# Kernel optimization log

Measured on AMD Instinct MI355X. Metric: run time of the kernel, lower is better.

## Reference

```python
import jax, jax.numpy as jnp
import numpy as np

B, T, L = 4096, 26, 4      # batch, num sparse tables, bag size (multi-hot)
N_ROWS, M = 100000, 64     # rows per table, embedding dim
LN_BOT = [13, 512, 256, 64]
LN_TOP = [415, 512, 256, 1]


def _mlp_params(key, ln):
    Ws, bs = [], []
    for i in range(len(ln) - 1):
        n, m = ln[i], ln[i + 1]
        key, k1, k2 = jax.random.split(key, 3)
        Ws.append(jax.random.normal(k1, (m, n), jnp.float32) * np.sqrt(2.0 / (m + n)))
        bs.append(jax.random.normal(k2, (m,), jnp.float32) * np.sqrt(1.0 / m))
    return Ws, bs


def setup_inputs() -> dict:
    key = jax.random.key(0)
    k_dense, k_idx, k_emb, k_bot, k_top = jax.random.split(key, 5)
    dense_x = jax.random.normal(k_dense, (B, LN_BOT[0]), jnp.float32)
    sparse_idx = jax.random.randint(k_idx, (B, T, L), 0, N_ROWS, jnp.int64 if jax.config.jax_enable_x64 else jnp.int32)
    # per-table uniform init U(-1/sqrt(n), 1/sqrt(n)); all tables same size -> stacked
    bound = np.sqrt(1.0 / N_ROWS)
    emb_tables = jax.random.uniform(k_emb, (T, N_ROWS, M), jnp.float32, -bound, bound)
    bw, bb = _mlp_params(k_bot, LN_BOT)
    tw, tb = _mlp_params(k_top, LN_TOP)
    return {
        "dense_x": dense_x, "sparse_idx": sparse_idx, "emb_tables": emb_tables,
        "bot_W0": bw[0], "bot_b0": bb[0], "bot_W1": bw[1], "bot_b1": bb[1],
        "bot_W2": bw[2], "bot_b2": bb[2],
        "top_W0": tw[0], "top_b0": tb[0], "top_W1": tw[1], "top_b1": tb[1],
        "top_W2": tw[2], "top_b2": tb[2],
    }


def _dlrm_forward(dense_x, sparse_idx, emb_tables, bot, top):
    # bottom MLP (all ReLU; sigmoid_layer index not hit for bottom)
    x = dense_x
    for W, b in bot:
        x = jax.nn.relu(x @ W.T + b)                       # [B, 64] at the end
    # apply_emb: per-table EmbeddingBag(mode='sum'): gather L rows, sum-pool
    # emb_tables: [T, N, M], sparse_idx: [B, T, L] -> E: [B, T, M]
    E = jax.vmap(lambda tab, ix: tab[ix].sum(axis=1), in_axes=(0, 1), out_axes=1)(
        emb_tables, sparse_idx)
    # dot interaction: concat bottom output with pooled embeddings
    Tcat = jnp.concatenate([x[:, None, :], E], axis=1)     # [B, T+1, M]
    Z = jnp.einsum("bim,bjm->bij", Tcat, Tcat)             # [B, T+1, T+1]
    li, lj = np.tril_indices(T + 1, k=-1)                  # strictly lower triangle
    Zflat = Z[:, li, lj]                                   # [B, (T+1)T/2]
    R = jnp.concatenate([x, Zflat], axis=1)                # [B, 415]
    # top MLP: ReLU hidden, Sigmoid on last layer
    h = R
    for i, (W, b) in enumerate(top):
        h = h @ W.T + b
        h = jax.nn.sigmoid(h) if i == len(top) - 1 else jax.nn.relu(h)
    return h                                               # [B, 1]


def reference(dense_x, sparse_idx, emb_tables,
              bot_W0, bot_b0, bot_W1, bot_b1, bot_W2, bot_b2,
              top_W0, top_b0, top_W1, top_b1, top_W2, top_b2):
    bot = [(bot_W0, bot_b0), (bot_W1, bot_b1), (bot_W2, bot_b2)]
    top = [(top_W0, top_b0), (top_W1, top_b1), (top_W2, top_b2)]
    return _dlrm_forward(dense_x, sparse_idx, emb_tables, bot, top)
```

## Files before the change

### kernel.cpp

```cpp
#include <hip/hip_runtime.h>
#include <hip/hip_bf16.h>
#include <cstddef>
#include <cstdint>

#define BATCH 4096
#define TT 26
#define LL 4
#define NROWS 100000
#define MM 64
#define RSTR 512

typedef __attribute__((ext_vector_type(8))) short bf16x8;
typedef __attribute__((ext_vector_type(4))) float f32x4;
typedef __attribute__((ext_vector_type(16))) float f32x16;

#define AS1 __attribute__((address_space(1)))
#define AS3 __attribute__((address_space(3)))

__device__ __forceinline__ void gload_lds16(const void* g, void* l) {
    __builtin_amdgcn_global_load_lds((const AS1 unsigned int*)g,
                                     (AS3 unsigned int*)l, 16, 0, 0);
}

__device__ __forceinline__ float bu2f(unsigned short u) {
    unsigned int x = (unsigned int)u << 16;
    float f; __builtin_memcpy(&f, &x, 4); return f;
}

#define CONVB 2112
__global__ __launch_bounds__(256) void gather_conv_kernel(
    const int* __restrict__ idx, const float* __restrict__ emb,
    const float* __restrict__ bw1, const float* __restrict__ bw2,
    const float* __restrict__ tw0, const float* __restrict__ tw1,
    __hip_bfloat16* __restrict__ bw1b, __hip_bfloat16* __restrict__ bw2b,
    __hip_bfloat16* __restrict__ tw0b, __hip_bfloat16* __restrict__ tw1b,
    unsigned short* __restrict__ E)
{
    __shared__ int sidx[TT * LL];
    const int tid = threadIdx.x;
    if (blockIdx.x < CONVB) {
        int i = blockIdx.x * 256 + tid;
        if (i < 131072) {
            bw1b[i] = __float2bfloat16(bw1[i]);
        } else if (i < 147456) {
            int j = i - 131072; bw2b[j] = __float2bfloat16(bw2[j]);
        } else if (i < 409600) {
            int j = i - 147456; int n = j >> 9, k = j & 511;
            tw0b[j] = __float2bfloat16(k < 415 ? tw0[n * 415 + k] : 0.f);
        } else {
            int j = i - 409600; tw1b[j] = __float2bfloat16(tw1[j]);
        }
        return;
    }
    const int b = blockIdx.x - CONVB;
    const int lane = tid & 63;
    const int w = tid >> 6;
    if (tid < TT * LL) sidx[tid] = idx[(size_t)b * (TT * LL) + tid];
    __syncthreads();

    float v[7][4];
#pragma unroll
    for (int rr = 0; rr < 7; rr++) {
        int t = rr * 4 + w;
        if (t < TT) {
            const float* tab = emb + (size_t)t * NROWS * MM + lane;
#pragma unroll
            for (int l = 0; l < LL; l++)
                v[rr][l] = tab[(size_t)sidx[t * LL + l] * MM];
        }
    }
#pragma unroll
    for (int rr = 0; rr < 7; rr++) {
        int t = rr * 4 + w;
        if (t < TT) {
            float s = v[rr][0] + v[rr][1] + v[rr][2] + v[rr][3];
            __hip_bfloat16 hv = __float2bfloat16(s);
            E[(size_t)b * (TT * MM) + t * MM + lane] = *(unsigned short*)&hv;
        }
    }
}

__global__ __launch_bounds__(256) void bottom_mlp_kernel(
    const float* __restrict__ dense, const float* __restrict__ bw0,
    const float* __restrict__ bb0,
    const __hip_bfloat16* __restrict__ w1b, const float* __restrict__ bb1,
    const __hip_bfloat16* __restrict__ w2b, const float* __restrict__ bb2,
    __hip_bfloat16* __restrict__ R)
{
    __shared__ float W0f[512 * 13];
    __shared__ float dL[16 * 13];
    __shared__ __align__(16) char x1L[16 * 1024];
    __shared__ __align__(16) char x2L[16 * 512];
    const int tid = threadIdx.x;
    const int lane = tid & 63;
    const int w = tid >> 6;
    const int b0 = blockIdx.x * 16;

    for (int i = tid; i < 512 * 13; i += 256) W0f[i] = bw0[i];
    if (tid < 208) dL[tid] = dense[(size_t)b0 * 13 + tid];
    __syncthreads();

    {
        const int m = tid & 15;
        float dv[13];
#pragma unroll
        for (int k = 0; k < 13; k++) dv[k] = dL[m * 13 + k];
#pragma unroll
        for (int j = 0; j < 32; j++) {
            int n = (tid >> 4) + j * 16;
            float s = bb0[n];
#pragma unroll
            for (int k = 0; k < 13; k++) s = fmaf(dv[k], W0f[n * 13 + k], s);
            __hip_bfloat16 hv = __float2bfloat16(fmaxf(s, 0.f));
            *(short*)(x1L + m * 1024 + ((n * 2) ^ ((m & 7) << 4))) = *(short*)&hv;
        }
    }
    __syncthreads();

    const int fr = lane & 15;
    const int fh = lane >> 4;

    {
        f32x4 acc1[4] = {};
#pragma unroll
        for (int kf = 0; kf < 16; kf++) {
            bf16x8 af = *(const bf16x8*)(x1L + fr * 1024 + ((kf * 64 + fh * 16) ^ ((fr & 7) << 4)));
#pragma unroll
            for (int nf = 0; nf < 4; nf++) {
                int n = w * 64 + nf * 16 + fr;
                bf16x8 bf = *(const bf16x8*)((const short*)w1b + (size_t)n * 512 + kf * 32 + fh * 8);
                acc1[nf] = __builtin_amdgcn_mfma_f32_16x16x32_bf16(af, bf, acc1[nf], 0, 0, 0);
            }
        }
#pragma unroll
        for (int nf = 0; nf < 4; nf++) {
            int n = w * 64 + nf * 16 + fr;
            float bias = bb1[n];
#pragma unroll
            for (int j = 0; j < 4; j++) {
                int m = fh * 4 + j;
                __hip_bfloat16 hv = __float2bfloat16(fmaxf(acc1[nf][j] + bias, 0.f));
                *(short*)(x2L + m * 512 + ((n * 2) ^ ((m & 7) << 4))) = *(short*)&hv;
            }
        }
    }
    __syncthreads();

    {
        f32x4 acc2 = {};
#pragma unroll
        for (int kf = 0; kf < 8; kf++) {
            bf16x8 af = *(const bf16x8*)(x2L + fr * 512 + ((kf * 64 + fh * 16) ^ ((fr & 7) << 4)));
            bf16x8 bf = *(const bf16x8*)((const short*)w2b + (size_t)(w * 16 + fr) * 256 + kf * 32 + fh * 8);
            acc2 = __builtin_amdgcn_mfma_f32_16x16x32_bf16(af, bf, acc2, 0, 0, 0);
        }
        int col = w * 16 + fr;
        float bias = bb2[col];
#pragma unroll
        for (int j = 0; j < 4; j++) {
            int m = fh * 4 + j;
            R[(size_t)(b0 + m) * RSTR + col] = __float2bfloat16(fmaxf(acc2[j] + bias, 0.f));
        }
    }
}

__global__ __launch_bounds__(256) void interact_kernel(
    const unsigned short* __restrict__ E, __hip_bfloat16* __restrict__ R)
{
    __shared__ __align__(16) char T[4][32 * 128];
    const int tid = threadIdx.x;
    const int lane = tid & 63;
    const int w = tid >> 6;
    const int b = blockIdx.x * 4 + w;
    char* Tw = T[w];
    const unsigned short* Eb = E + (size_t)b * (TT * MM);
    const unsigned short* Xb = (const unsigned short*)R + (size_t)b * RSTR;

#pragma unroll
    for (int i = 0; i < 7; i++) {
        int id = i * 64 + lane;
        if (id < 432) {
            int r = id >> 4, c4 = (id & 15) * 4;
            const unsigned short* src = (r == 0) ? (Xb + c4) : (Eb + (r - 1) * 64 + c4);
            ushort4 val = *(const ushort4*)src;
            *(ushort4*)(Tw + r * 128 + ((c4 * 2) ^ ((r & 7) << 4))) = val;
        }
    }
#pragma unroll
    for (int i = 0; i < 2; i++) {
        int id = i * 64 + lane;
        if (id < 80) {
            int r = 27 + (id >> 4), c4 = (id & 15) * 4;
            *(ushort4*)(Tw + r * 128 + ((c4 * 2) ^ ((r & 7) << 4))) = (ushort4){0, 0, 0, 0};
        }
    }
    __syncthreads();

    f32x16 acc = {};
#pragma unroll
    for (int m = 0; m < 4; m++) {
        int byteoff = (lane & 31) * 128 + ((m * 32 + (lane >> 5) * 16) ^ ((lane & 7) << 4));
        bf16x8 f = *(const bf16x8*)(Tw + byteoff);
        acc = __builtin_amdgcn_mfma_f32_32x32x16_bf16(f, f, acc, 0, 0, 0);
    }
    __hip_bfloat16* Rb = R + (size_t)b * RSTR;
    const int col = lane & 31;
#pragma unroll
    for (int q = 0; q < 4; q++) {
#pragma unroll
        for (int j = 0; j < 4; j++) {
            int row = j + 8 * q + 4 * (lane >> 5);
            if (row < 27 && col < row)
                Rb[64 + row * (row - 1) / 2 + col] = __float2bfloat16(acc[q * 4 + j]);
        }
    }
    for (int p = lane; p < 97; p += 64)
        Rb[415 + p] = __float2bfloat16(0.f);
}

template<int KK, int ACT>
__global__ __launch_bounds__(256) void gemm_fullk(
    const __hip_bfloat16* __restrict__ A,
    const __hip_bfloat16* __restrict__ W,
    const float* __restrict__ bias,
    __hip_bfloat16* __restrict__ C, int ldc)
{
    constexpr int HS   = KK / 2;
    constexpr int CPRH = KK / 16;
    constexpr int NI   = (64 * CPRH) / 256;
    __shared__ __align__(16) short As0[64 * HS];
    __shared__ __align__(16) short As1[64 * HS];
    __shared__ __align__(16) short Bs0[64 * HS];
    __shared__ __align__(16) short Bs1[64 * HS];

    const int tid  = threadIdx.x;
    const int lane = tid & 63;
    const int wid  = tid >> 6;
    const int wr   = wid >> 1, wc = wid & 1;

    const char* Ab = (const char*)A + (size_t)blockIdx.x * (64 * KK * 2);
    const char* Wb = (const char*)W + (size_t)blockIdx.y * (64 * KK * 2);

    auto stage = [&](const char* Gb, short* Ls, int h) {
#pragma unroll
        for (int j = 0; j < NI; j++) {
            int ci  = j * 256 + tid;
            int row = ci / CPRH;
            int cb  = (ci & (CPRH - 1)) * 16;
            int src = row * (2 * KK) + h * KK + (cb ^ ((row & 7) << 4));
            gload_lds16(Gb + src, (char*)Ls + row * KK + cb);
        }
    };
    stage(Ab, As0, 0); stage(Wb, Bs0, 0);
    stage(Ab, As1, 1); stage(Wb, Bs1, 1);

    const int frow = lane & 15;
    const int fkb  = (lane >> 4) * 16;
    const int xr   = (frow & 7) << 4;
    const int oA0  = (wr * 32 + frow) * KK;
    const int oA1  = oA0 + 16 * KK;
    const int oB0  = (wc * 32 + frow) * KK;
    const int oB1  = oB0 + 16 * KK;

    f32x4 acc[2][2] = {};

    auto compute = [&](const short* Ah, const short* Bh) {
#pragma unroll
        for (int ks = 0; ks < KK / 64; ks++) {
            int pc = (ks * 64 + fkb) ^ xr;
            bf16x8 a0 = *(const bf16x8*)((const char*)Ah + oA0 + pc);
            bf16x8 a1 = *(const bf16x8*)((const char*)Ah + oA1 + pc);
            bf16x8 b0 = *(const bf16x8*)((const char*)Bh + oB0 + pc);
            bf16x8 b1 = *(const bf16x8*)((const char*)Bh + oB1 + pc);
            acc[0][0] = __builtin_amdgcn_mfma_f32_16x16x32_bf16(a0, b0, acc[0][0], 0, 0, 0);
            acc[0][1] = __builtin_amdgcn_mfma_f32_16x16x32_bf16(a0, b1, acc[0][1], 0, 0, 0);
            acc[1][0] = __builtin_amdgcn_mfma_f32_16x16x32_bf16(a1, b0, acc[1][0], 0, 0, 0);
            acc[1][1] = __builtin_amdgcn_mfma_f32_16x16x32_bf16(a1, b1, acc[1][1], 0, 0, 0);
        }
    };

    asm volatile("s_waitcnt vmcnt(%0)" :: "i"(2 * NI) : "memory");
    __builtin_amdgcn_sched_barrier(0);
    __builtin_amdgcn_s_barrier();
    __builtin_amdgcn_sched_barrier(0);
    compute(As0, Bs0);
    asm volatile("s_waitcnt vmcnt(0)" ::: "memory");
    __builtin_amdgcn_sched_barrier(0);
    __builtin_amdgcn_s_barrier();
    __builtin_amdgcn_sched_barrier(0);
    compute(As1, Bs1);

    const int col0 = blockIdx.y * 64 + wc * 32 + (lane & 15);
    const int row0 = blockIdx.x * 64 + wr * 32 + (lane >> 4) * 4;
    float bias_n0 = bias[col0];
    float bias_n1 = bias[col0 + 16];
#pragma unroll
    for (int mi = 0; mi < 2; mi++) {
#pragma unroll
        for (int j = 0; j < 4; j++) {
            int row = row0 + mi * 16 + j;
            float v0 = acc[mi][0][j] + bias_n0;
            float v1 = acc[mi][1][j] + bias_n1;
            if (ACT == 1) { v0 = fmaxf(v0, 0.f); v1 = fmaxf(v1, 0.f); }
            C[(size_t)row * ldc + col0]      = __float2bfloat16(v0);
            C[(size_t)row * ldc + col0 + 16] = __float2bfloat16(v1);
        }
    }
}

__global__ __launch_bounds__(256) void top2_kernel(
    const __hip_bfloat16* __restrict__ h, const float* __restrict__ W,
    const float* __restrict__ bias, float* __restrict__ out)
{
    __shared__ float ws[256];
    int tid = threadIdx.x;
    ws[tid] = W[tid];
    __syncthreads();
    int b = blockIdx.x * 4 + (tid >> 6);
    int lane = tid & 63;
    const unsigned short* hb = (const unsigned short*)(h + (size_t)b * 256);
    ushort4 hv = *(const ushort4*)&hb[lane * 4];
    float4 wv = *(const float4*)&ws[lane * 4];
    float s = bu2f(hv.x) * wv.x + bu2f(hv.y) * wv.y + bu2f(hv.z) * wv.z + bu2f(hv.w) * wv.w;
#pragma unroll
    for (int off = 32; off >= 1; off >>= 1)
        s += __shfl_xor(s, off, 64);
    if (lane == 0) {
        float v = s + bias[0];
        out[b] = 1.0f / (1.0f + expf(-v));
    }
}

extern "C" void kernel_launch(void* const* d_in, const int* in_sizes, int n_in,
                              void* d_out, int out_size, void* d_ws, size_t ws_size,
                              hipStream_t stream) {
    const float* dense = (const float*)d_in[0];
    const int*   sidx  = (const int*)d_in[1];
    const float* emb   = (const float*)d_in[2];
    const float* bw0   = (const float*)d_in[3];
    const float* bb0   = (const float*)d_in[4];
    const float* bw1   = (const float*)d_in[5];
    const float* bb1   = (const float*)d_in[6];
    const float* bw2   = (const float*)d_in[7];
    const float* bb2   = (const float*)d_in[8];
    const float* tw0   = (const float*)d_in[9];
    const float* tb0   = (const float*)d_in[10];
    const float* tw1   = (const float*)d_in[11];
    const float* tb1   = (const float*)d_in[12];
    const float* tw2   = (const float*)d_in[13];
    const float* tb2   = (const float*)d_in[14];
    float* out = (float*)d_out;

    char* wsb = (char*)d_ws;
    unsigned short* E    = (unsigned short*)(wsb);
    __hip_bfloat16* R    = (__hip_bfloat16*)(wsb + (16u << 20));
    __hip_bfloat16* h1   = (__hip_bfloat16*)(wsb + (20u << 20));
    __hip_bfloat16* h2   = (__hip_bfloat16*)(wsb + (24u << 20));
    __hip_bfloat16* bw1b = (__hip_bfloat16*)(wsb + (26u << 20));
    __hip_bfloat16* bw2b = bw1b + 131072;
    __hip_bfloat16* tw0b = bw2b + 16384;
    __hip_bfloat16* tw1b = tw0b + 262144;

    gather_conv_kernel<<<CONVB + BATCH, 256, 0, stream>>>(
        sidx, emb, bw1, bw2, tw0, tw1, bw1b, bw2b, tw0b, tw1b, E);

    bottom_mlp_kernel<<<BATCH / 16, 256, 0, stream>>>(
        dense, bw0, bb0, bw1b, bb1, bw2b, bb2, R);

    interact_kernel<<<BATCH / 4, 256, 0, stream>>>(E, R);

    gemm_fullk<512, 1><<<dim3(64, 8), 256, 0, stream>>>(R, tw0b, tb0, h1, 512);

    gemm_fullk<512, 1><<<dim3(64, 4), 256, 0, stream>>>(h1, tw1b, tb1, h2, 256);

    top2_kernel<<<BATCH / 4, 256, 0, stream>>>(h2, tw2, tb2, out);
}
```

Measured before the change: 61.00 us.

## Split bottom MLP into fused front kernel plus double-buffered LDS GEMMs

Replaces the per-16-row bottom MLP kernel with three parts. The first layer is folded into the gather/convert front kernel, one block per sample, writing x1 to global memory. Layers two and three then run on a new K-step double-buffered LDS GEMM, which also replaces the full-K GEMM used by the top MLP. The aim is to stop re-reading the bottom weights from global memory per 16-row block and to cut LDS footprint (launch_bounds 256,2) for better occupancy. The cost is an extra kernel launch, x1/x2 round-trips through global memory, and only 64 blocks for the last bottom layer.

```diff
diff --git a/kernel.cpp b/kernel.cpp
--- a/kernel.cpp
+++ b/kernel.cpp
@@ -27,19 +27,65 @@
     float f; __builtin_memcpy(&f, &x, 4); return f;
 }
 
-#define CONVB 2112
-__global__ __launch_bounds__(256) void gather_conv_kernel(
+#define GATB 4096
+#define BOT0B 8192
+__global__ __launch_bounds__(256) void fused_front_kernel(
     const int* __restrict__ idx, const float* __restrict__ emb,
+    const float* __restrict__ dense, const float* __restrict__ bw0,
+    const float* __restrict__ bb0,
     const float* __restrict__ bw1, const float* __restrict__ bw2,
     const float* __restrict__ tw0, const float* __restrict__ tw1,
+    unsigned short* __restrict__ E, __hip_bfloat16* __restrict__ x1,
     __hip_bfloat16* __restrict__ bw1b, __hip_bfloat16* __restrict__ bw2b,
-    __hip_bfloat16* __restrict__ tw0b, __hip_bfloat16* __restrict__ tw1b,
-    unsigned short* __restrict__ E)
+    __hip_bfloat16* __restrict__ tw0b, __hip_bfloat16* __restrict__ tw1b)
 {
     __shared__ int sidx[TT * LL];
+    __shared__ float xr[13];
     const int tid = threadIdx.x;
-    if (blockIdx.x < CONVB) {
-        int i = blockIdx.x * 256 + tid;
+
+    if (blockIdx.x < GATB) {
+        const int b = blockIdx.x;
+        const int lane = tid & 63;
+        const int w = tid >> 6;
+        if (tid < TT * LL) sidx[tid] = idx[(size_t)b * (TT * LL) + tid];
+        __syncthreads();
+        float v[7][4];
+#pragma unroll
+        for (int rr = 0; rr < 7; rr++) {
+            int t = rr * 4 + w;
+            if (t < TT) {
+                const float* tab = emb + (size_t)t * NROWS * MM + lane;
+#pragma unroll
+                for (int l = 0; l < LL; l++)
+                    v[rr][l] = tab[(size_t)sidx[t * LL + l] * MM];
+            }
+        }
+#pragma unroll
+        for (int rr = 0; rr < 7; rr++) {
+            int t = rr * 4 + w;
+            if (t < TT) {
+                float s = v[rr][0] + v[rr][1] + v[rr][2] + v[rr][3];
+                __hip_bfloat16 hv = __float2bfloat16(s);
+                E[(size_t)b * (TT * MM) + t * MM + lane] = *(unsigned short*)&hv;
+            }
+        }
+        return;
+    }
+    if (blockIdx.x < BOT0B) {
+        const int b = blockIdx.x - GATB;
+        if (tid < 13) xr[tid] = dense[b * 13 + tid];
+        __syncthreads();
+        for (int j = tid; j < 512; j += 256) {
+            const float* w = bw0 + j * 13;
+            float s = bb0[j];
+#pragma unroll
+            for (int k = 0; k < 13; k++) s = fmaf(xr[k], w[k], s);
+            x1[(size_t)b * 512 + j] = __float2bfloat16(fmaxf(s, 0.f));
+        }
+        return;
+    }
+    {
+        int i = (blockIdx.x - BOT0B) * 256 + tid;
         if (i < 131072) {
             bw1b[i] = __float2bfloat16(bw1[i]);
         } else if (i < 147456) {
@@ -47,119 +93,100 @@
         } else if (i < 409600) {
             int j = i - 147456; int n = j >> 9, k = j & 511;
             tw0b[j] = __float2bfloat16(k < 415 ? tw0[n * 415 + k] : 0.f);
-        } else {
+        } else if (i < 540672) {
             int j = i - 409600; tw1b[j] = __float2bfloat16(tw1[j]);
         }
-        return;
-    }
-    const int b = blockIdx.x - CONVB;
+    }
+}
+
+template<int KK, int ACT>
+__global__ __launch_bounds__(256, 2) void gemm_db(
+    const __hip_bfloat16* __restrict__ A,
+    const __hip_bfloat16* __restrict__ W,
+    const float* __restrict__ bias,
+    __hip_bfloat16* __restrict__ C, int ldc)
+{
+    constexpr int KSTEPS = KK / 128;
+    __shared__ __align__(16) short As[2][64 * 128];
+    __shared__ __align__(16) short Bs[2][64 * 128];
+
+    const int tid  = threadIdx.x;
     const int lane = tid & 63;
-    const int w = tid >> 6;
-    if (tid < TT * LL) sidx[tid] = idx[(size_t)b * (TT * LL) + tid];
-    __syncthreads();
-
-    float v[7][4];
-#pragma unroll
-    for (int rr = 0; rr < 7; rr++) {
-        int t = rr * 4 + w;
-        if (t < TT) {
-            const float* tab = emb + (size_t)t * NROWS * MM + lane;
-#pragma unroll
-            for (int l = 0; l < LL; l++)
-                v[rr][l] = tab[(size_t)sidx[t * LL + l] * MM];
-        }
-    }
-#pragma unroll
-    for (int rr = 0; rr < 7; rr++) {
-        int t = rr * 4 + w;
-        if (t < TT) {
-            float s = v[rr][0] + v[rr][1] + v[rr][2] + v[rr][3];
-            __hip_bfloat16 hv = __float2bfloat16(s);
-            E[(size_t)b * (TT * MM) + t * MM + lane] = *(unsigned short*)&hv;
-        }
-    }
-}
-
-__global__ __launch_bounds__(256) void bottom_mlp_kernel(
-    const float* __restrict__ dense, const float* __restrict__ bw0,
-    const float* __restrict__ bb0,
-    const __hip_bfloat16* __restrict__ w1b, const float* __restrict__ bb1,
-    const __hip_bfloat16* __restrict__ w2b, const float* __restrict__ bb2,
-    __hip_bfloat16* __restrict__ R)
-{
-    __shared__ float W0f[512 * 13];
-    __shared__ float dL[16 * 13];
-    __shared__ __align__(16) char x1L[16 * 1024];
-    __shared__ __align__(16) char x2L[16 * 512];
-    const int tid = threadIdx.x;
-    const int lane = tid & 63;
-    const int w = tid >> 6;
-    const int b0 = blockIdx.x * 16;
-
-    for (int i = tid; i < 512 * 13; i += 256) W0f[i] = bw0[i];
-    if (tid < 208) dL[tid] = dense[(size_t)b0 * 13 + tid];
-    __syncthreads();
-
-    {
-        const int m = tid & 15;
-        float dv[13];
-#pragma unroll
-        for (int k = 0; k < 13; k++) dv[k] = dL[m * 13 + k];
-#pragma unroll
-        for (int j = 0; j < 32; j++) {
-            int n = (tid >> 4) + j * 16;
-            float s = bb0[n];
-#pragma unroll
-            for (int k = 0; k < 13; k++) s = fmaf(dv[k], W0f[n * 13 + k], s);
-            __hip_bfloat16 hv = __float2bfloat16(fmaxf(s, 0.f));
-            *(short*)(x1L + m * 1024 + ((n * 2) ^ ((m & 7) << 4))) = *(short*)&hv;
-        }
-    }
-    __syncthreads();
-
-    const int fr = lane & 15;
-    const int fh = lane >> 4;
-
-    {
-        f32x4 acc1[4] = {};
-#pragma unroll
-        for (int kf = 0; kf < 16; kf++) {
-            bf16x8 af = *(const bf16x8*)(x1L + fr * 1024 + ((kf * 64 + fh * 16) ^ ((fr & 7) << 4)));
-#pragma unroll
-            for (int nf = 0; nf < 4; nf++) {
-                int n = w * 64 + nf * 16 + fr;
-                bf16x8 bf = *(const bf16x8*)((const short*)w1b + (size_t)n * 512 + kf * 32 + fh * 8);
-                acc1[nf] = __builtin_amdgcn_mfma_f32_16x16x32_bf16(af, bf, acc1[nf], 0, 0, 0);
-            }
-        }
-#pragma unroll
-        for (int nf = 0; nf < 4; nf++) {
-            int n = w * 64 + nf * 16 + fr;
-            float bias = bb1[n];
-#pragma unroll
-            for (int j = 0; j < 4; j++) {
-                int m = fh * 4 + j;
-                __hip_bfloat16 hv = __float2bfloat16(fmaxf(acc1[nf][j] + bias, 0.f));
-                *(short*)(x2L + m * 512 + ((n * 2) ^ ((m & 7) << 4))) = *(short*)&hv;
-            }
-        }
-    }
-    __syncthreads();
-
-    {
-        f32x4 acc2 = {};
-#pragma unroll
-        for (int kf = 0; kf < 8; kf++) {
-            bf16x8 af = *(const bf16x8*)(x2L + fr * 512 + ((kf * 64 + fh * 16) ^ ((fr & 7) << 4)));
-            bf16x8 bf = *(const bf16x8*)((const short*)w2b + (size_t)(w * 16 + fr) * 256 + kf * 32 + fh * 8);
-            acc2 = __builtin_amdgcn_mfma_f32_16x16x32_bf16(af, bf, acc2, 0, 0, 0);
-        }
-        int col = w * 16 + fr;
-        float bias = bb2[col];
+    const int wid  = tid >> 6;
+    const int wr   = wid >> 1, wc = wid & 1;
+
+    const char* Ab = (const char*)A + (size_t)blockIdx.x * (64 * KK * 2);
+    const char* Wb = (const char*)W + (size_t)blockIdx.y * (64 * KK * 2);
+
+    auto stage = [&](const char* Gb, char* Ls, int ks) {
 #pragma unroll
         for (int j = 0; j < 4; j++) {
-            int m = fh * 4 + j;
-            R[(size_t)(b0 + m) * RSTR + col] = __float2bfloat16(fmaxf(acc2[j] + bias, 0.f));
+            int ci  = j * 256 + tid;
+            int row = ci >> 4;
+            int cb  = (ci & 15) * 16;
+            int src = row * (2 * KK) + ks * 256 + (cb ^ ((row & 7) << 4));
+            gload_lds16(Gb + src, Ls + row * 256 + cb);
+        }
+    };
+
+    const int fr  = lane & 15;
+    const int fkb = (lane >> 4) * 16;
+    const int xrr = (fr & 7) << 4;
+    const int oA0 = (wr * 32 + fr) * 256;
+    const int oA1 = oA0 + 16 * 256;
+    const int oB0 = (wc * 32 + fr) * 256;
+    const int oB1 = oB0 + 16 * 256;
+
+    f32x4 acc[2][2] = {};
+
+    auto compute = [&](const char* Ah, const char* Bh) {
+#pragma unroll
+        for (int kf = 0; kf < 4; kf++) {
+            int pc = (kf * 64 + fkb) ^ xrr;
+            bf16x8 a0 = *(const bf16x8*)(Ah + oA0 + pc);
+            bf16x8 a1 = *(const bf16x8*)(Ah + oA1 + pc);
+            bf16x8 b0 = *(const bf16x8*)(Bh + oB0 + pc);
+            bf16x8 b1 = *(const bf16x8*)(Bh + oB1 + pc);
+            acc[0][0] = __builtin_amdgcn_mfma_f32_16x16x32_bf16(a0, b0, acc[0][0], 0, 0, 0);
+            acc[0][1] = __builtin_amdgcn_mfma_f32_16x16x32_bf16(a0, b1, acc[0][1], 0, 0, 0);
+            acc[1][0] = __builtin_amdgcn_mfma_f32_16x16x32_bf16(a1, b0, acc[1][0], 0, 0, 0);
+            acc[1][1] = __builtin_amdgcn_mfma_f32_16x16x32_bf16(a1, b1, acc[1][1], 0, 0, 0);
+        }
+    };
+
+    stage(Ab, (char*)As[0], 0); stage(Wb, (char*)Bs[0], 0);
+    stage(Ab, (char*)As[1], 1); stage(Wb, (char*)Bs[1], 1);
+
+#pragma unroll
+    for (int ks = 0; ks < KSTEPS; ks++) {
+        if (ks < KSTEPS - 1) { asm volatile("s_waitcnt vmcnt(8)" ::: "memory"); }
+        else                 { asm volatile("s_waitcnt vmcnt(0)" ::: "memory"); }
+        __builtin_amdgcn_sched_barrier(0);
+        __builtin_amdgcn_s_barrier();
+        __builtin_amdgcn_sched_barrier(0);
+        compute((const char*)As[ks & 1], (const char*)Bs[ks & 1]);
+        __builtin_amdgcn_sched_barrier(0);
+        if (ks + 2 < KSTEPS) {
+            __builtin_amdgcn_s_barrier();
+            stage(Ab, (char*)As[ks & 1], ks + 2);
+            stage(Wb, (char*)Bs[ks & 1], ks + 2);
+        }
+    }
+
+    const int col0 = blockIdx.y * 64 + wc * 32 + (lane & 15);
+    const int row0 = blockIdx.x * 64 + wr * 32 + (lane >> 4) * 4;
+    float bias_n0 = bias[col0];
+    float bias_n1 = bias[col0 + 16];
+#pragma unroll
+    for (int mi = 0; mi < 2; mi++) {
+#pragma unroll
+        for (int j = 0; j < 4; j++) {
+            int row = row0 + mi * 16 + j;
+            float v0 = acc[mi][0][j] + bias_n0;
+            float v1 = acc[mi][1][j] + bias_n1;
+            if (ACT == 1) { v0 = fmaxf(v0, 0.f); v1 = fmaxf(v1, 0.f); }
+            C[(size_t)row * ldc + col0]      = __float2bfloat16(v0);
+            C[(size_t)row * ldc + col0 + 16] = __float2bfloat16(v1);
         }
     }
 }
@@ -216,96 +243,6 @@
     }
     for (int p = lane; p < 97; p += 64)
         Rb[415 + p] = __float2bfloat16(0.f);
-}
-
-template<int KK, int ACT>
-__global__ __launch_bounds__(256) void gemm_fullk(
-    const __hip_bfloat16* __restrict__ A,
-    const __hip_bfloat16* __restrict__ W,
-    const float* __restrict__ bias,
-    __hip_bfloat16* __restrict__ C, int ldc)
-{
-    constexpr int HS   = KK / 2;
-    constexpr int CPRH = KK / 16;
-    constexpr int NI   = (64 * CPRH) / 256;
-    __shared__ __align__(16) short As0[64 * HS];
-    __shared__ __align__(16) short As1[64 * HS];
-    __shared__ __align__(16) short Bs0[64 * HS];
-    __shared__ __align__(16) short Bs1[64 * HS];
-
-    const int tid  = threadIdx.x;
-    const int lane = tid & 63;
-    const int wid  = tid >> 6;
-    const int wr   = wid >> 1, wc = wid & 1;
-
-    const char* Ab = (const char*)A + (size_t)blockIdx.x * (64 * KK * 2);
-    const char* Wb = (const char*)W + (size_t)blockIdx.y * (64 * KK * 2);
-
-    auto stage = [&](const char* Gb, short* Ls, int h) {
-#pragma unroll
-        for (int j = 0; j < NI; j++) {
-            int ci  = j * 256 + tid;
-            int row = ci / CPRH;
-            int cb  = (ci & (CPRH - 1)) * 16;
-            int src = row * (2 * KK) + h * KK + (cb ^ ((row & 7) << 4));
-            gload_lds16(Gb + src, (char*)Ls + row * KK + cb);
-        }
-    };
-    stage(Ab, As0, 0); stage(Wb, Bs0, 0);
-    stage(Ab, As1, 1); stage(Wb, Bs1, 1);
-
-    const int frow = lane & 15;
-    const int fkb  = (lane >> 4) * 16;
-    const int xr   = (frow & 7) << 4;
-    const int oA0  = (wr * 32 + frow) * KK;
-    const int oA1  = oA0 + 16 * KK;
-    const int oB0  = (wc * 32 + frow) * KK;
-    const int oB1  = oB0 + 16 * KK;
-
-    f32x4 acc[2][2] = {};
-
-    auto compute = [&](const short* Ah, const short* Bh) {
-#pragma unroll
-        for (int ks = 0; ks < KK / 64; ks++) {
-            int pc = (ks * 64 + fkb) ^ xr;
-            bf16x8 a0 = *(const bf16x8*)((const char*)Ah + oA0 + pc);
-            bf16x8 a1 = *(const bf16x8*)((const char*)Ah + oA1 + pc);
-            bf16x8 b0 = *(const bf16x8*)((const char*)Bh + oB0 + pc);
-            bf16x8 b1 = *(const bf16x8*)((const char*)Bh + oB1 + pc);
-            acc[0][0] = __builtin_amdgcn_mfma_f32_16x16x32_bf16(a0, b0, acc[0][0], 0, 0, 0);
-            acc[0][1] = __builtin_amdgcn_mfma_f32_16x16x32_bf16(a0, b1, acc[0][1], 0, 0, 0);
-            acc[1][0] = __builtin_amdgcn_mfma_f32_16x16x32_bf16(a1, b0, acc[1][0], 0, 0, 0);
-            acc[1][1] = __builtin_amdgcn_mfma_f32_16x16x32_bf16(a1, b1, acc[1][1], 0, 0, 0);
-        }
-    };
-
-    asm volatile("s_waitcnt vmcnt(%0)" :: "i"(2 * NI) : "memory");
-    __builtin_amdgcn_sched_barrier(0);
-    __builtin_amdgcn_s_barrier();
-    __builtin_amdgcn_sched_barrier(0);
-    compute(As0, Bs0);
-    asm volatile("s_waitcnt vmcnt(0)" ::: "memory");
-    __builtin_amdgcn_sched_barrier(0);
-    __builtin_amdgcn_s_barrier();
-    __builtin_amdgcn_sched_barrier(0);
-    compute(As1, Bs1);
-
-    const int col0 = blockIdx.y * 64 + wc * 32 + (lane & 15);
-    const int row0 = blockIdx.x * 64 + wr * 32 + (lane >> 4) * 4;
-    float bias_n0 = bias[col0];
-    float bias_n1 = bias[col0 + 16];
-#pragma unroll
-    for (int mi = 0; mi < 2; mi++) {
-#pragma unroll
-        for (int j = 0; j < 4; j++) {
-            int row = row0 + mi * 16 + j;
-            float v0 = acc[mi][0][j] + bias_n0;
-            float v1 = acc[mi][1][j] + bias_n1;
-            if (ACT == 1) { v0 = fmaxf(v0, 0.f); v1 = fmaxf(v1, 0.f); }
-            C[(size_t)row * ldc + col0]      = __float2bfloat16(v0);
-            C[(size_t)row * ldc + col0 + 16] = __float2bfloat16(v1);
-        }
-    }
 }
 
 __global__ __launch_bounds__(256) void top2_kernel(
@@ -356,22 +293,26 @@
     __hip_bfloat16* R    = (__hip_bfloat16*)(wsb + (16u << 20));
     __hip_bfloat16* h1   = (__hip_bfloat16*)(wsb + (20u << 20));
     __hip_bfloat16* h2   = (__hip_bfloat16*)(wsb + (24u << 20));
-    __hip_bfloat16* bw1b = (__hip_bfloat16*)(wsb + (26u << 20));
+    __hip_bfloat16* x1   = (__hip_bfloat16*)(wsb + (26u << 20));
+    __hip_bfloat16* x2   = (__hip_bfloat16*)(wsb + (30u << 20));
+    __hip_bfloat16* bw1b = (__hip_bfloat16*)(wsb + (32u << 20));
     __hip_bfloat16* bw2b = bw1b + 131072;
     __hip_bfloat16* tw0b = bw2b + 16384;
     __hip_bfloat16* tw1b = tw0b + 262144;
 
-    gather_conv_kernel<<<CONVB + BATCH, 256, 0, stream>>>(
-        sidx, emb, bw1, bw2, tw0, tw1, bw1b, bw2b, tw0b, tw1b, E);
-
-    bottom_mlp_kernel<<<BATCH / 16, 256, 0, stream>>>(
-        dense, bw0, bb0, bw1b, bb1, bw2b, bb2, R);
+    fused_front_kernel<<<GATB + BATCH + 2112, 256, 0, stream>>>(
+        sidx, emb, dense, bw0, bb0, bw1, bw2, tw0, tw1,
+        E, x1, bw1b, bw2b, tw0b, tw1b);
+
+    gemm_db<512, 1><<<dim3(64, 4), 256, 0, stream>>>(x1, bw1b, bb1, x2, 256);
+
+    gemm_db<256, 1><<<dim3(64, 1), 256, 0, stream>>>(x2, bw2b, bb2, R, RSTR);
 
     interact_kernel<<<BATCH / 4, 256, 0, stream>>>(E, R);
 
-    gemm_fullk<512, 1><<<dim3(64, 8), 256, 0, stream>>>(R, tw0b, tb0, h1, 512);
-
-    gemm_fullk<512, 1><<<dim3(64, 4), 256, 0, stream>>>(h1, tw1b, tb1, h2, 256);
+    gemm_db<512, 1><<<dim3(64, 8), 256, 0, stream>>>(R, tw0b, tb0, h1, 512);
+
+    gemm_db<512, 1><<<dim3(64, 4), 256, 0, stream>>>(h1, tw1b, tb1, h2, 256);
 
     top2_kernel<<<BATCH / 4, 256, 0, stream>>>(h2, tw2, tb2, out);
 }
```

Result: faster. 56.79 us (-6.9%).
